# Optimization experiments

Measured on AMD Instinct MI355X. Metric: run time of the kernel, lower is better.

Reference implementation:

```python
import jax, jax.numpy as jnp
import numpy as np

HIDDEN = 50


def _lstm_layer(x_tbi, w_ih, w_hh, b_ih, b_hh):
    """One LSTM layer, PyTorch gate order (i, f, g, o).
    x_tbi: [T, B, in]; returns h sequence [T, B, H]."""
    B = x_tbi.shape[1]
    H = w_hh.shape[1]
    # Precompute input projections for all timesteps at once (one big GEMM).
    x_proj = jnp.einsum('tbi,gi->tbg', x_tbi, w_ih) + b_ih + b_hh  # [T, B, 4H]

    def step(carry, xp):
        h, c = carry
        gates = xp + h @ w_hh.T  # [B, 4H]
        i, f, g, o = jnp.split(gates, 4, axis=-1)
        i = jax.nn.sigmoid(i)
        f = jax.nn.sigmoid(f)
        g = jnp.tanh(g)
        o = jax.nn.sigmoid(o)
        c = f * c + i * g
        h = o * jnp.tanh(c)
        return (h, c), h

    h0 = jnp.zeros((B, H), dtype=x_tbi.dtype)
    c0 = jnp.zeros((B, H), dtype=x_tbi.dtype)
    _, hs = jax.lax.scan(step, (h0, c0), x_proj)
    return hs  # [T, B, H]


def setup_inputs() -> dict:
    key = jax.random.key(0)
    ks = jax.random.split(key, 12)
    B, T, I, H = 2048, 512, 12, HIDDEN
    s_in = 1.0 / np.sqrt(H)  # PyTorch LSTM init scale
    inp = {
        'x': jax.random.normal(ks[0], (B, T, I), dtype=jnp.float32),
        'w_ih0': jax.random.uniform(ks[1], (4 * H, I), jnp.float32, -s_in, s_in),
        'w_hh0': jax.random.uniform(ks[2], (4 * H, H), jnp.float32, -s_in, s_in),
        'b_ih0': jax.random.uniform(ks[3], (4 * H,), jnp.float32, -s_in, s_in),
        'b_hh0': jax.random.uniform(ks[4], (4 * H,), jnp.float32, -s_in, s_in),
        'w_ih1': jax.random.uniform(ks[5], (4 * H, H), jnp.float32, -s_in, s_in),
        'w_hh1': jax.random.uniform(ks[6], (4 * H, H), jnp.float32, -s_in, s_in),
        'b_ih1': jax.random.uniform(ks[7], (4 * H,), jnp.float32, -s_in, s_in),
        'b_hh1': jax.random.uniform(ks[8], (4 * H,), jnp.float32, -s_in, s_in),
        'w_out': jax.random.uniform(ks[9], (1, H), jnp.float32, -s_in, s_in),
        'b_out': jax.random.uniform(ks[10], (1,), jnp.float32, -s_in, s_in),
    }
    return inp


def reference(x, w_ih0, w_hh0, b_ih0, b_hh0, w_ih1, w_hh1, b_ih1, b_hh1, w_out, b_out):
    # x: [B, T, I] (batch_first). Scan works over leading time axis.
    x_tbi = jnp.transpose(x, (1, 0, 2))  # [T, B, I]
    h1 = _lstm_layer(x_tbi, w_ih0, w_hh0, b_ih0, b_hh0)  # [T, B, H]
    h2 = _lstm_layer(h1, w_ih1, w_hh1, b_ih1, b_hh1)     # [T, B, H]
    last = h2[-1]                                         # r_out[:, -1, :] -> [B, H]
    logits = last @ w_out.T + b_out                       # [B, 1]
    return jax.nn.sigmoid(logits)
```

## Files before the change

kernel.cpp:

```cpp
#include <hip/hip_runtime.h>

#define TT   512
#define BI   12
#define HH   50
#define BB   8
#define BTOT 2048
#define LOG2E 1.4426950408889634f


typedef _Float16 half8 __attribute__((ext_vector_type(8)));
typedef float    f4    __attribute__((ext_vector_type(4)));

__device__ __forceinline__ float sigm_(float v) {
    return __builtin_amdgcn_rcpf(1.f + __builtin_amdgcn_exp2f(v * (-LOG2E)));
}
__device__ __forceinline__ float tanh_(float v) {
    return 1.f - 2.f * __builtin_amdgcn_rcpf(1.f + __builtin_amdgcn_exp2f(v * (2.f * LOG2E)));
}
__device__ __forceinline__ float dppmerge_(float a0, float a1) {
    int r = __builtin_amdgcn_update_dpp(__builtin_bit_cast(int, a0),
                                        __builtin_bit_cast(int, a1),
                                        0x128, 0xF, 0xC, false);
    return __builtin_bit_cast(float, r);
}

__launch_bounds__(1024)
__global__ void lstm2_kernel(const float* __restrict__ x,
                             const float* __restrict__ w_ih0, const float* __restrict__ w_hh0,
                             const float* __restrict__ b_ih0, const float* __restrict__ b_hh0,
                             const float* __restrict__ w_ih1, const float* __restrict__ w_hh1,
                             const float* __restrict__ b_ih1, const float* __restrict__ b_hh1,
                             const float* __restrict__ w_out, const float* __restrict__ b_out,
                             float* __restrict__ out)
{
    const int tid   = threadIdx.x;
    const int wv    = tid >> 6;
    const int lane  = tid & 63;
    const int layer = wv >> 3;
    const int w8    = wv & 7;
    const int b0    = blockIdx.x * BB;
    const int t0     = (w8 < 5) ? 2 * w8 : (5 + w8);
    const int ntiles = (w8 < 5) ? 2 : 1;

    __shared__ __align__(16) _Float16 B0s[2][64  * 16];
    __shared__ __align__(16) _Float16 B1s[2][128 * 16];

    const int m = lane & 15;
    const int q = lane >> 4;
    half8 af[2][4];
    #pragma unroll
    for (int s = 0; s < 2; s++) {
        #pragma unroll
        for (int kb = 0; kb < 4; kb++) {
            #pragma unroll
            for (int j = 0; j < 8; j++) {
                float v = 0.f;
                if (s < ntiles && (layer == 1 || kb < 2)) {
                    const int T  = t0 + s;
                    const int u  = T * 4 + (m >> 2);
                    const int g  = m & 3;
                    const int kg = kb * 32 + q * 8 + j;
                    if (u < HH) {
                        const int r = g * HH + u;
                        if (layer == 0) {
                            if      (kg < 12)  v = w_ih0[r * BI + kg];
                            else if (kg < 62)  v = w_hh0[r * HH + (kg - 12)];
                            else if (kg == 62) v = b_ih0[r] + b_hh0[r];
                        } else {
                            if      (kg < 50)  v = w_ih1[r * HH + kg];
                            else if (kg < 64)  v = 0.f;
                            else if (kg < 114) v = w_hh1[r * HH + (kg - 64)];
                            else if (kg == 114) v = b_ih1[r] + b_hh1[r];
                        }
                    }
                }
                af[s][kb][j] = (_Float16)v;
            }
        }
    }

    for (int i = tid; i < 2 * 64 * 16;  i += 1024) (&B0s[0][0])[i] = (_Float16)0.f;
    for (int i = tid; i < 2 * 128 * 16; i += 1024) (&B1s[0][0])[i] = (_Float16)0.f;
    __syncthreads();
    if (tid < 16) {
        B0s[0][7  * 128 + tid * 8 + 6] = (_Float16)1.f;
        B0s[1][7  * 128 + tid * 8 + 6] = (_Float16)1.f;
        B1s[0][14 * 128 + tid * 8 + 2] = (_Float16)1.f;
        B1s[1][14 * 128 + tid * 8 + 2] = (_Float16)1.f;
    }
    const int xb = tid / 12, xi = tid - xb * 12;
    const int xoff = (xi >> 3) * 128 + xb * 8 + (xi & 7);
    const size_t xbase = ((size_t)(b0 + xb) * TT) * BI + xi;
    if (tid < 96)
        B0s[0][xoff] = (_Float16)x[xbase];
    __syncthreads();

    const int n16  = lane & 15;
    const int slot = n16 >> 3;
    const int bcol = n16 & 7;
    const int u_m  = (t0 + slot) * 4 + q;
    const bool wvalid = (u_m < HH) && (slot == 0 || ntiles == 2);
    float cm = 0.f;

    const _Float16* rdA[2] = { (layer ? &B1s[0][0] : &B0s[0][0]) + lane * 8,
                               (layer ? &B1s[1][0] : &B0s[1][0]) + lane * 8 };
    const int k0 = 12 + u_m;
    const int k1 = 64 + u_m;
    const int offA = layer ? ((k1 >> 3) * 128 + bcol * 8 + (k1 & 7))
                           : ((k0 >> 3) * 128 + bcol * 8 + (k0 & 7));
    const int offB = (u_m >> 3) * 128 + bcol * 8 + (u_m & 7);
    _Float16* wAp[2] = { (layer ? &B1s[0][0] : &B0s[0][0]) + offA,
                         (layer ? &B1s[1][0] : &B0s[1][0]) + offA };
    _Float16* wBp[2] = { &B1s[0][0] + offB, &B1s[1][0] + offB };
    _Float16* xdp[2] = { &B0s[0][0] + xoff, &B0s[1][0] + xoff };

    const float* xq = x + xbase + BI;

#define STEP(P, DOL0, DOL1, DOX)                                              \
  {                                                                           \
    float xpre = 0.f;                                                         \
    if ((DOX) && tid < 96) xpre = *xq;                                        \
    if ((layer == 0) ? (DOL0) : (DOL1)) {                                     \
      f4 acc0 = {0.f, 0.f, 0.f, 0.f}, acc1 = {0.f, 0.f, 0.f, 0.f};            \
      const _Float16* Bp = rdA[P];                                            \
      if (layer == 0) {                                                       \
        _Pragma("unroll")                                                     \
        for (int kb = 0; kb < 2; kb++) {                                      \
          const half8 bf = *(const half8*)(Bp + kb * 512);                    \
          acc0 = __builtin_amdgcn_mfma_f32_16x16x32_f16(af[0][kb], bf, acc0, 0, 0, 0); \
          if (ntiles > 1)                                                     \
            acc1 = __builtin_amdgcn_mfma_f32_16x16x32_f16(af[1][kb], bf, acc1, 0, 0, 0); \
        }                                                                     \
      } else {                                                                \
        _Pragma("unroll")                                                     \
        for (int kb = 0; kb < 4; kb++) {                                      \
          const half8 bf = *(const half8*)(Bp + kb * 512);                    \
          acc0 = __builtin_amdgcn_mfma_f32_16x16x32_f16(af[0][kb], bf, acc0, 0, 0, 0); \
          if (ntiles > 1)                                                     \
            acc1 = __builtin_amdgcn_mfma_f32_16x16x32_f16(af[1][kb], bf, acc1, 0, 0, 0); \
        }                                                                     \
      }                                                                       \
      f4 am;                                                                  \
      _Pragma("unroll")                                                       \
      for (int i = 0; i < 4; i++) am[i] = dppmerge_(acc0[i], acc1[i]);        \
      const float iv = sigm_(am[0]);                                          \
      const float fv = sigm_(am[1]);                                          \
      const float gv = tanh_(am[2]);                                          \
      const float ov = sigm_(am[3]);                                          \
      cm = fv * cm + iv * gv;                                                 \
      const float h = ov * tanh_(cm);                                         \
      if (wvalid) {                                                           \
        const _Float16 hh = (_Float16)h;                                      \
        *wAp[1 - (P)] = hh;                                                   \
        if (layer == 0) *wBp[1 - (P)] = hh;                                   \
      }                                                                       \
    }                                                                         \
    if ((DOX) && tid < 96) *xdp[1 - (P)] = (_Float16)xpre;                    \
    if (DOX) xq += BI;                                                        \
    __syncthreads();                                                          \
  }

    STEP(0, 1, 0, 1)
    STEP(1, 1, 1, 1)
    #pragma unroll 1
    for (int it = 0; it < 254; ++it) {
        STEP(0, 1, 1, 1)
        STEP(1, 1, 1, 1)
    }
    STEP(0, 1, 1, 1)
    STEP(1, 1, 1, 0)
    STEP(0, 0, 1, 0)
#undef STEP

    if (tid < BB) {
        float s = b_out[0];
        #pragma unroll
        for (int u = 0; u < HH; u++) {
            const int kk = 64 + u;
            s += w_out[u] * (float)B1s[1][(kk >> 3) * 128 + tid * 8 + (kk & 7)];
        }
        out[b0 + tid] = sigm_(s);
    }
}

extern "C" void kernel_launch(void* const* d_in, const int* in_sizes, int n_in,
                              void* d_out, int out_size, void* d_ws, size_t ws_size,
                              hipStream_t stream) {
    const float* x     = (const float*)d_in[0];
    const float* w_ih0 = (const float*)d_in[1];
    const float* w_hh0 = (const float*)d_in[2];
    const float* b_ih0 = (const float*)d_in[3];
    const float* b_hh0 = (const float*)d_in[4];
    const float* w_ih1 = (const float*)d_in[5];
    const float* w_hh1 = (const float*)d_in[6];
    const float* b_ih1 = (const float*)d_in[7];
    const float* b_hh1 = (const float*)d_in[8];
    const float* w_out = (const float*)d_in[9];
    const float* b_out = (const float*)d_in[10];
    float* out = (float*)d_out;

    dim3 grid(BTOT / BB);
    dim3 block(1024);
    lstm2_kernel<<<grid, block, 0, stream>>>(x, w_ih0, w_hh0, b_ih0, b_hh0,
                                             w_ih1, w_hh1, b_ih1, b_hh1,
                                             w_out, b_out, out);
}
```

Before: 397.4 us.

## Halve batch per block to 4 and use 4 waves per layer with 4 MFMA tiles

Reduces the batch columns per block from 8 to 4 and the threads per block from 1024 to 512, so each layer runs on 4 waves that each handle up to 4 gate tiles instead of 2. A three-level DPP select merges the four accumulators into per-lane gate values. The grid doubles to 512 blocks with a launch-bound hint for several resident blocks per CU, so more independent blocks can overlap their serial recurrence. In exchange each MFMA carries more zero padding, since only 4 of the 16 B columns hold real batch, and each wave issues more sequential MFMAs per timestep.

Measured after the change: 488.6 us. +22.9%, slower.

```diff
diff --git a/kernel.cpp b/kernel.cpp
--- a/kernel.cpp
+++ b/kernel.cpp
@@ -3,7 +3,7 @@
 #define TT   512
 #define BI   12
 #define HH   50
-#define BB   8
+#define BB   4
 #define BTOT 2048
 #define LOG2E 1.4426950408889634f
 
@@ -17,14 +17,15 @@
 __device__ __forceinline__ float tanh_(float v) {
     return 1.f - 2.f * __builtin_amdgcn_rcpf(1.f + __builtin_amdgcn_exp2f(v * (2.f * LOG2E)));
 }
-__device__ __forceinline__ float dppmerge_(float a0, float a1) {
-    int r = __builtin_amdgcn_update_dpp(__builtin_bit_cast(int, a0),
-                                        __builtin_bit_cast(int, a1),
-                                        0x128, 0xF, 0xC, false);
+template <int CTRL, int BANK>
+__device__ __forceinline__ float dppsel_(float o, float s) {
+    int r = __builtin_amdgcn_update_dpp(__builtin_bit_cast(int, o),
+                                        __builtin_bit_cast(int, s),
+                                        CTRL, 0xF, BANK, false);
     return __builtin_bit_cast(float, r);
 }
 
-__launch_bounds__(1024)
+__launch_bounds__(512, 4)
 __global__ void lstm2_kernel(const float* __restrict__ x,
                              const float* __restrict__ w_ih0, const float* __restrict__ w_hh0,
                              const float* __restrict__ b_ih0, const float* __restrict__ b_hh0,
@@ -36,27 +37,26 @@
     const int tid   = threadIdx.x;
     const int wv    = tid >> 6;
     const int lane  = tid & 63;
-    const int layer = wv >> 3;
-    const int w8    = wv & 7;
+    const int layer = wv >> 2;
+    const int wl    = wv & 3;
     const int b0    = blockIdx.x * BB;
-    const int t0     = (w8 < 5) ? 2 * w8 : (5 + w8);
-    const int ntiles = (w8 < 5) ? 2 : 1;
+    const int ntile = (wl == 0) ? 4 : 3;
 
     __shared__ __align__(16) _Float16 B0s[2][64  * 16];
     __shared__ __align__(16) _Float16 B1s[2][128 * 16];
 
     const int m = lane & 15;
     const int q = lane >> 4;
-    half8 af[2][4];
+    half8 af[4][4];
     #pragma unroll
-    for (int s = 0; s < 2; s++) {
+    for (int s = 0; s < 4; s++) {
+        const int T = wl + 4 * s;
         #pragma unroll
         for (int kb = 0; kb < 4; kb++) {
             #pragma unroll
             for (int j = 0; j < 8; j++) {
                 float v = 0.f;
-                if (s < ntiles && (layer == 1 || kb < 2)) {
-                    const int T  = t0 + s;
+                if (s < ntile && (layer == 1 || kb < 2)) {
                     const int u  = T * 4 + (m >> 2);
                     const int g  = m & 3;
                     const int kg = kb * 32 + q * 8 + j;
@@ -79,8 +79,8 @@
         }
     }
 
-    for (int i = tid; i < 2 * 64 * 16;  i += 1024) (&B0s[0][0])[i] = (_Float16)0.f;
-    for (int i = tid; i < 2 * 128 * 16; i += 1024) (&B1s[0][0])[i] = (_Float16)0.f;
+    for (int i = tid; i < 2 * 64 * 16;  i += 512) (&B0s[0][0])[i] = (_Float16)0.f;
+    for (int i = tid; i < 2 * 128 * 16; i += 512) (&B1s[0][0])[i] = (_Float16)0.f;
     __syncthreads();
     if (tid < 16) {
         B0s[0][7  * 128 + tid * 8 + 6] = (_Float16)1.f;
@@ -91,15 +91,16 @@
     const int xb = tid / 12, xi = tid - xb * 12;
     const int xoff = (xi >> 3) * 128 + xb * 8 + (xi & 7);
     const size_t xbase = ((size_t)(b0 + xb) * TT) * BI + xi;
-    if (tid < 96)
+    if (tid < 48)
         B0s[0][xoff] = (_Float16)x[xbase];
     __syncthreads();
 
     const int n16  = lane & 15;
-    const int slot = n16 >> 3;
-    const int bcol = n16 & 7;
-    const int u_m  = (t0 + slot) * 4 + q;
-    const bool wvalid = (u_m < HH) && (slot == 0 || ntiles == 2);
+    const int slot = n16 >> 2;
+    const int bcol = n16 & 3;
+    const int Ts   = wl + 4 * slot;
+    const int u_m  = Ts * 4 + q;
+    const bool wvalid = (Ts <= 12) && (u_m < HH);
     float cm = 0.f;
 
     const _Float16* rdA[2] = { (layer ? &B1s[0][0] : &B0s[0][0]) + lane * 8,
@@ -119,30 +120,38 @@
 #define STEP(P, DOL0, DOL1, DOX)                                              \
   {                                                                           \
     float xpre = 0.f;                                                         \
-    if ((DOX) && tid < 96) xpre = *xq;                                        \
+    if ((DOX) && tid < 48) xpre = *xq;                                        \
     if ((layer == 0) ? (DOL0) : (DOL1)) {                                     \
-      f4 acc0 = {0.f, 0.f, 0.f, 0.f}, acc1 = {0.f, 0.f, 0.f, 0.f};            \
+      f4 acc[4];                                                              \
+      _Pragma("unroll")                                                       \
+      for (int s = 0; s < 4; s++) acc[s] = (f4){0.f, 0.f, 0.f, 0.f};          \
       const _Float16* Bp = rdA[P];                                            \
       if (layer == 0) {                                                       \
         _Pragma("unroll")                                                     \
         for (int kb = 0; kb < 2; kb++) {                                      \
           const half8 bf = *(const half8*)(Bp + kb * 512);                    \
-          acc0 = __builtin_amdgcn_mfma_f32_16x16x32_f16(af[0][kb], bf, acc0, 0, 0, 0); \
-          if (ntiles > 1)                                                     \
-            acc1 = __builtin_amdgcn_mfma_f32_16x16x32_f16(af[1][kb], bf, acc1, 0, 0, 0); \
+          _Pragma("unroll")                                                   \
+          for (int s = 0; s < 4; s++)                                         \
+            if (s < ntile)                                                    \
+              acc[s] = __builtin_amdgcn_mfma_f32_16x16x32_f16(af[s][kb], bf, acc[s], 0, 0, 0); \
         }                                                                     \
       } else {                                                                \
         _Pragma("unroll")                                                     \
         for (int kb = 0; kb < 4; kb++) {                                      \
           const half8 bf = *(const half8*)(Bp + kb * 512);                    \
-          acc0 = __builtin_amdgcn_mfma_f32_16x16x32_f16(af[0][kb], bf, acc0, 0, 0, 0); \
-          if (ntiles > 1)                                                     \
-            acc1 = __builtin_amdgcn_mfma_f32_16x16x32_f16(af[1][kb], bf, acc1, 0, 0, 0); \
+          _Pragma("unroll")                                                   \
+          for (int s = 0; s < 4; s++)                                         \
+            if (s < ntile)                                                    \
+              acc[s] = __builtin_amdgcn_mfma_f32_16x16x32_f16(af[s][kb], bf, acc[s], 0, 0, 0); \
         }                                                                     \
       }                                                                       \
       f4 am;                                                                  \
       _Pragma("unroll")                                                       \
-      for (int i = 0; i < 4; i++) am[i] = dppmerge_(acc0[i], acc1[i]);        \
+      for (int i = 0; i < 4; i++) {                                           \
+        float t1 = dppsel_<0x12C, 0x2>(acc[0][i], acc[1][i]);                 \
+        float t2 = dppsel_<0x128, 0x4>(t1, acc[2][i]);                        \
+        am[i]    = dppsel_<0x124, 0x8>(t2, acc[3][i]);                        \
+      }                                                                       \
       const float iv = sigm_(am[0]);                                          \
       const float fv = sigm_(am[1]);                                          \
       const float gv = tanh_(am[2]);                                          \
@@ -155,7 +164,7 @@
         if (layer == 0) *wBp[1 - (P)] = hh;                                   \
       }                                                                       \
     }                                                                         \
-    if ((DOX) && tid < 96) *xdp[1 - (P)] = (_Float16)xpre;                    \
+    if ((DOX) && tid < 48) *xdp[1 - (P)] = (_Float16)xpre;                    \
     if (DOX) xq += BI;                                                        \
     __syncthreads();                                                          \
   }
@@ -200,7 +209,7 @@
     float* out = (float*)d_out;
 
     dim3 grid(BTOT / BB);
-    dim3 block(1024);
+    dim3 block(512);
     lstm2_kernel<<<grid, block, 0, stream>>>(x, w_ih0, w_hh0, b_ih0, b_hh0,
                                              w_ih1, w_hh1, b_ih1, b_hh1,
                                              w_out, b_out, out);
```
